# Performance work log

Hardware: AMD Instinct MI355X
Metric: run time of the kernel (lower is better)

## Reference

```python
import jax, jax.numpy as jnp
import numpy as np

V, E, H1, H2, B, T = 50000, 256, 512, 512, 512, 80

def setup_inputs() -> dict:
    key = jax.random.key(0)
    ks = jax.random.split(key, 10)
    s = lambda fan: 1.0 / np.sqrt(fan)
    return {
        "tokens": jax.random.randint(ks[0], (B, T), 0, V),
        "emb": jax.random.normal(ks[1], (V, E), jnp.float32) * 0.05,
        "W1": jax.random.normal(ks[2], (E, 4 * H1), jnp.float32) * s(E),
        "U1": jax.random.normal(ks[3], (H1, 4 * H1), jnp.float32) * s(H1),
        "b1": jnp.zeros((4 * H1,), jnp.float32),
        "W2": jax.random.normal(ks[4], (H1, 4 * H2), jnp.float32) * s(H1),
        "U2": jax.random.normal(ks[5], (H2, 4 * H2), jnp.float32) * s(H2),
        "b2": jnp.zeros((4 * H2,), jnp.float32),
        "Wfc": jax.random.normal(ks[6], (H2, 1), jnp.float32) * s(H2),
        "bfc": jnp.zeros((1,), jnp.float32),
    }

def _lstm_step(x, h, c, W, U, b):
    # z: [B, 4H] in Keras gate order i, f, g(cell), o
    z = x @ W + h @ U + b
    i, f, g, o = jnp.split(z, 4, axis=-1)
    c_new = jax.nn.sigmoid(f) * c + jax.nn.sigmoid(i) * jnp.tanh(g)
    h_new = jax.nn.sigmoid(o) * jnp.tanh(c_new)
    return h_new, c_new

def reference(tokens, emb, W1, U1, b1, W2, U2, b2, Wfc, bfc):
    X = emb[tokens]                    # [B, T, E]
    Xt = jnp.swapaxes(X, 0, 1)         # [T, B, E] for scan over time
    Bsz = tokens.shape[0]
    init = (jnp.zeros((Bsz, H1), X.dtype), jnp.zeros((Bsz, H1), X.dtype),
            jnp.zeros((Bsz, H2), X.dtype), jnp.zeros((Bsz, H2), X.dtype))

    def step(carry, x):
        h1, c1, h2, c2 = carry
        h1, c1 = _lstm_step(x, h1, c1, W1, U1, b1)
        h2, c2 = _lstm_step(h1, h2, c2, W2, U2, b2)
        return (h1, c1, h2, c2), None

    (h1, c1, h2, c2), _ = jax.lax.scan(step, init, Xt)
    # Dense(1) on last-step layer-2 output, then sigmoid (dropout inactive at inference)
    return jax.nn.sigmoid(h2 @ Wfc + bfc)   # [B, 1]
```

## Files before the change

### kernel.cpp

```cpp
#include <hip/hip_runtime.h>
#include <hip/hip_bf16.h>

typedef __bf16  bf16x8 __attribute__((ext_vector_type(8)));
typedef float   f32x4  __attribute__((ext_vector_type(4)));

#define GLOAD16_C(gptr, lptr) \
  __builtin_amdgcn_global_load_lds((const __attribute__((address_space(1))) void*)(gptr), \
                                   (__attribute__((address_space(3))) void*)(lptr), 16, 0, 0)
#define GLOAD16_H(gptr, lptr) \
  __builtin_amdgcn_global_load_lds((const __attribute__((address_space(1))) void*)(gptr), \
                                   (__attribute__((address_space(3))) void*)(lptr), 16, 0, 0x1)

#define WAIT_VM10  asm volatile("s_waitcnt vmcnt(10)" ::: "memory")
#define WAIT_VM8   asm volatile("s_waitcnt vmcnt(8)"  ::: "memory")
#define WAIT_VM6   asm volatile("s_waitcnt vmcnt(6)"  ::: "memory")
#define WAIT_VM4   asm volatile("s_waitcnt vmcnt(4)"  ::: "memory")
#define WAIT_VM2   asm volatile("s_waitcnt vmcnt(2)"  ::: "memory")
#define WAIT_VM0   asm volatile("s_waitcnt vmcnt(0)"  ::: "memory")

__device__ __forceinline__ void wait_vm_chunks(int n) {
  if      (n <= 0) WAIT_VM0;
  else if (n == 1) WAIT_VM2;
  else if (n == 2) WAIT_VM4;
  else if (n == 3) WAIT_VM6;
  else if (n == 4) WAIT_VM8;
  else             WAIT_VM10;
}
__device__ __forceinline__ void wait_lgkm_n(int n) {
  if      (n <= 0) asm volatile("s_waitcnt lgkmcnt(0)" ::: "memory");
  else if (n <= 2) asm volatile("s_waitcnt lgkmcnt(2)" ::: "memory");
  else             asm volatile("s_waitcnt lgkmcnt(6)" ::: "memory");
}

__device__ __forceinline__ float sigm(float x)  { return 1.0f / (1.0f + __expf(-x)); }
__device__ __forceinline__ float tanhp(float x) { return 2.0f / (1.0f + __expf(-2.0f * x)) - 1.0f; }

__device__ __forceinline__ unsigned int coh_load(const unsigned int* p) {
  unsigned int v;
  asm volatile("global_load_dword %0, %1, off sc0 sc1\n\ts_waitcnt vmcnt(0)"
               : "=v"(v) : "v"(p) : "memory");
  return v;
}
__device__ __forceinline__ int coh_load_i(const int* p) {
  int v;
  asm volatile("global_load_dword %0, %1, off sc0 sc1\n\ts_waitcnt vmcnt(0)"
               : "=v"(v) : "v"(p) : "memory");
  return v;
}
__device__ __forceinline__ void coh_store16(void* p, bf16x8 v) {
  f32x4 f = *(f32x4*)&v;
  asm volatile("global_store_dwordx4 %0, %1, off sc0 sc1" :: "v"(p), "v"(f) : "memory");
}
__device__ __forceinline__ void flag_store(int* fp, int v) {
  asm volatile("global_store_dword %0, %1, off sc0 sc1" :: "v"(fp), "v"(v) : "memory");
}

#define TSTEPS 80
#define BATCH  512
#define EDIM   256
#define HDIM   512
#define K2     1024
#define K1     768
#define NCH    16
#define D_SLOTS 12
#define SLOT_BYTES 524544
#define RING_OFF 65536
#define EPI_OFF  131072
#define EPI_STR  24
#define LDS_BYTES 137216

struct Params {
  const __hip_bfloat16* Wz1t;
  const __hip_bfloat16* Wz2t;
  const float* bz1;
  const float* bz2;
  const __hip_bfloat16* Xall;
  char* h1base;
  char* h2base;
  int* flags;
  const float* Wfc; const float* bfc;
  float* out;
};


__global__ __launch_bounds__(256) void prep_weights(
    const float* __restrict__ W1, const float* __restrict__ U1, const float* __restrict__ b1,
    const float* __restrict__ W2, const float* __restrict__ U2, const float* __restrict__ b2,
    __hip_bfloat16* __restrict__ Wz1t, __hip_bfloat16* __restrict__ Wz2t,
    float* __restrict__ bz1, float* __restrict__ bz2) {
  long idx = (long)blockIdx.x * 256 + threadIdx.x;
  const long n1 = 2048L * K1, n2 = 2048L * K2;
  if (idx < n1) {
    int n = (int)(idx / K1), k = (int)(idx % K1);
    int col = ((n >> 4) & 3) * 512 + (n >> 6) * 16 + (n & 15);
    float v = (k < 256) ? W1[(size_t)k * 2048 + col] : U1[(size_t)(k - 256) * 2048 + col];
    Wz1t[idx] = __float2bfloat16(v);
  } else if (idx < n1 + n2) {
    long r = idx - n1;
    int n = (int)(r / K2), k = (int)(r % K2);
    int col = ((n >> 4) & 3) * 512 + (n >> 6) * 16 + (n & 15);
    float v = (k < 512) ? W2[(size_t)k * 2048 + col] : U2[(size_t)(k - 512) * 2048 + col];
    Wz2t[r] = __float2bfloat16(v);
  } else if (idx < n1 + n2 + 2048) {
    int n = (int)(idx - (n1 + n2));
    bz1[n] = b1[((n >> 4) & 3) * 512 + (n >> 6) * 16 + (n & 15)];
  } else if (idx < n1 + n2 + 4096) {
    int n = (int)(idx - (n1 + n2 + 2048));
    bz2[n] = b2[((n >> 4) & 3) * 512 + (n >> 6) * 16 + (n & 15)];
  }
}

__global__ __launch_bounds__(256) void prep_gather(
    const int* __restrict__ tokens, const float* __restrict__ emb,
    __hip_bfloat16* __restrict__ Xall, float4* __restrict__ zp, int zn) {
  int idx = blockIdx.x * 256 + threadIdx.x;
  if (idx < zn) zp[idx] = make_float4(0.f, 0.f, 0.f, 0.f);
  int e  = (idx & 63) * 4;
  int rb = idx >> 6;
  int t  = rb >> 9;
  int b  = rb & 511;
  int tok = tokens[b * TSTEPS + t];
  const float4 v = *(const float4*)&emb[(size_t)tok * EDIM + e];
  __hip_bfloat16* o = Xall + (size_t)rb * EDIM + e;
  o[0] = __float2bfloat16(v.x); o[1] = __float2bfloat16(v.y);
  o[2] = __float2bfloat16(v.z); o[3] = __float2bfloat16(v.w);
}


__device__ __forceinline__ void gate_wave(const int* flags, int base1, int t1,
                                          int base2, int t2, int lane) {
  const int idx = lane & 31;
  const int* fp = flags + (((lane < 32) ? base1 : base2) + idx) * 4;
  const int tgt = (lane < 32) ? t1 : t2;
  for (;;) {
    int v = coh_load_i(fp);
    if (__ballot(v >= tgt) == ~0ull) break;
    __builtin_amdgcn_s_sleep(2);
  }
}

template<int K0, int LEN, int STRIDE, bool COH>
__device__ __forceinline__ void run_part(
    const __hip_bfloat16* __restrict__ Asrc, int m0, int w, int lane,
    __hip_bfloat16* __restrict__ ring, const __hip_bfloat16* __restrict__ BsL,
    const bf16x8 (&breg)[NCH][4], const int (&aoff)[2], const int (&boff)[4],
    f32x4 (&acc)[2][4]) {
  auto stage = [&](int kc) {
#pragma unroll
    for (int it = 0; it < 2; ++it) {
      const int gbase = w * 128 + it * 64;
      const int g   = gbase + lane;
      const int row = g >> 2;
      const int gc  = (g & 3) ^ ((row >> 1) & 3);
      __hip_bfloat16* lp = ring + (kc & 7) * 4096 + gbase * 8;
      const __hip_bfloat16* gp = Asrc + (size_t)(m0 + row) * STRIDE + (kc - K0) * 32 + gc * 8;
      if (COH) GLOAD16_H(gp, lp); else GLOAD16_C(gp, lp);
    }
  };
#pragma unroll
  for (int f = 0; f < 6; ++f) stage(K0 + f);

  bf16x8 af[2][2], bf[2][4];
  wait_vm_chunks(5);
#pragma unroll
  for (int mi = 0; mi < 2; ++mi)
    af[0][mi] = *(const bf16x8*)(ring + (K0 & 7) * 4096 + aoff[mi]);
  if (K0 >= NCH)
#pragma unroll
    for (int g = 0; g < 4; ++g)
      bf[0][g] = *(const bf16x8*)(BsL + (K0 - NCH) * 2048 + boff[g]);

#pragma unroll
  for (int i = 0; i < LEN; ++i) {
    const int kc  = K0 + i;
    const int cur = i & 1, nxt = cur ^ 1;
    if (i + 1 < LEN) {
      wait_vm_chunks(LEN - 2 - i < 4 ? LEN - 2 - i : 4);
      const int kn = kc + 1;
#pragma unroll
      for (int mi = 0; mi < 2; ++mi)
        af[nxt][mi] = *(const bf16x8*)(ring + (kn & 7) * 4096 + aoff[mi]);
      if (kn >= NCH) {
#pragma unroll
        for (int g = 0; g < 4; ++g)
          bf[nxt][g] = *(const bf16x8*)(BsL + (kn - NCH) * 2048 + boff[g]);
        wait_lgkm_n(6);
      } else {
        wait_lgkm_n(2);
      }
      if (i + 6 < LEN) stage(kc + 6);
    } else {
      wait_lgkm_n(0);
    }
#pragma unroll
    for (int mi = 0; mi < 2; ++mi)
#pragma unroll
      for (int g = 0; g < 4; ++g)
        acc[mi][g] = __builtin_amdgcn_mfma_f32_16x16x32_bf16(
            af[cur][mi], (kc < NCH ? breg[kc][g] : bf[cur][g]), acc[mi][g], 0, 0, 0);
  }
}

template<bool Z2>
__device__ __forceinline__ void role_loop(const Params& p, char* smem, int tid,
                                          int grp, int ntile) {
  constexpr int K   = Z2 ? K2 : K1;
  constexpr int NC  = K / 32;
  constexpr int NCA = Z2 ? 16 : 8;
  const int lane = tid & 63;
  const int w    = tid >> 6;
  const int q    = lane >> 4;
  const int m16  = lane & 15;
  const int m0   = grp * 128;
  const int n0   = ntile * 64;

  __hip_bfloat16* BsL  = (__hip_bfloat16*)smem;
  __hip_bfloat16* ring = (__hip_bfloat16*)(smem + RING_OFF);
  __hip_bfloat16* epi  = (__hip_bfloat16*)(smem + EPI_OFF);

  const __hip_bfloat16* Bg = (Z2 ? p.Wz2t : p.Wz1t) + (size_t)n0 * K;

  bf16x8 breg[NCH][4];
#pragma unroll
  for (int kc = 0; kc < NCH; ++kc)
#pragma unroll
    for (int g = 0; g < 4; ++g)
      breg[kc][g] = *(const bf16x8*)(Bg + (size_t)(g * 16 + m16) * K + kc * 32 + q * 8);

  for (int it0 = tid; it0 < (NC - NCH) * 256; it0 += 256) {
    int cid = it0 >> 8, gg = it0 & 255;
    int r = gg >> 2, c8 = gg & 3;
    int sw = c8 ^ ((r >> 1) & 3);
    *(bf16x8*)(BsL + cid * 2048 + r * 32 + sw * 8) =
        *(const bf16x8*)(Bg + (size_t)r * K + (NCH + cid) * 32 + c8 * 8);
  }
  const float* bias = Z2 ? p.bz2 : p.bz1;
  float bz[4];
#pragma unroll
  for (int g = 0; g < 4; ++g) bz[g] = bias[n0 + g * 16 + m16];

  const int swz = (q ^ ((m16 >> 1) & 3)) * 8;
  int aoff[2], boff[4];
#pragma unroll
  for (int mi = 0; mi < 2; ++mi) aoff[mi] = (w * 32 + mi * 16 + m16) * 32 + swz;
#pragma unroll
  for (int g = 0; g < 4; ++g)    boff[g]  = (g * 16 + m16) * 32 + swz;

  float cst[2][4] = {{0.f,0.f,0.f,0.f},{0.f,0.f,0.f,0.f}};
  const int fself = (Z2 ? 128 : 0) + grp * 32 + ntile;
  const int jbase = ntile * 16;
  __syncthreads();

  for (int s = 0; s < TSTEPS; ++s) {
    const int sl = s % D_SLOTS, slp = (s + D_SLOTS - 1) % D_SLOTS;
    const __hip_bfloat16* Aa = Z2
        ? (const __hip_bfloat16*)(p.h1base + (size_t)sl * SLOT_BYTES)
        : p.Xall + (size_t)s * BATCH * EDIM;
    const __hip_bfloat16* Ab = Z2
        ? (const __hip_bfloat16*)(p.h2base + (size_t)slp * SLOT_BYTES)
        : (const __hip_bfloat16*)(p.h1base + (size_t)slp * SLOT_BYTES);
    __hip_bfloat16* hout = (__hip_bfloat16*)
        ((Z2 ? p.h2base : p.h1base) + (size_t)sl * SLOT_BYTES);

    f32x4 acc[2][4];
#pragma unroll
    for (int mi = 0; mi < 2; ++mi)
#pragma unroll
      for (int g = 0; g < 4; ++g)
        acc[mi][g] = (f32x4){bz[g], bz[g], bz[g], bz[g]};

    if (Z2) {
      if (w == 0) gate_wave(p.flags, grp * 32, s + 1, grp * 32, s + 1, lane);
      __syncthreads();
    }
    if (Z2) run_part<0, 16, 512, true >(Aa, m0, w, lane, ring, BsL, breg, aoff, boff, acc);
    else    run_part<0,  8, 256, false>(Aa, m0, w, lane, ring, BsL, breg, aoff, boff, acc);

    if (w == 0) {
      if (Z2) gate_wave(p.flags, 128 + grp * 32, s, 128 + grp * 32, s, lane);
      else    gate_wave(p.flags, grp * 32, s, 128 + grp * 32, s - (D_SLOTS - 1), lane);
      if ((s & 7) == 0) __builtin_amdgcn_fence(__ATOMIC_ACQUIRE, "agent");
    }
    __syncthreads();
    if (Z2) run_part<16, 16, 512, true>(Ab, m0, w, lane, ring, BsL, breg, aoff, boff, acc);
    else    run_part< 8, 16, 512, true>(Ab, m0, w, lane, ring, BsL, breg, aoff, boff, acc);

#pragma unroll
    for (int mi = 0; mi < 2; ++mi)
#pragma unroll
      for (int rr = 0; rr < 4; ++rr) {
        const float zi = acc[mi][0][rr], zf = acc[mi][1][rr];
        const float zg = acc[mi][2][rr], zo = acc[mi][3][rr];
        const float cn = sigm(zf) * cst[mi][rr] + sigm(zi) * tanhp(zg);
        cst[mi][rr] = cn;
        epi[(w * 32 + mi * 16 + q * 4 + rr) * EPI_STR + m16] = __float2bfloat16(sigm(zo) * tanhp(cn));
      }
    __syncthreads();
    {
      const int r = tid >> 1, hf = tid & 1;
      bf16x8 hv = *(const bf16x8*)(epi + r * EPI_STR + hf * 8);
      coh_store16(hout + (size_t)(m0 + r) * HDIM + jbase + hf * 8, hv);
    }
    WAIT_VM0;
    __syncthreads();
    if (tid == 0) flag_store(p.flags + fself * 4, s + 1);
  }
}

__global__ __launch_bounds__(256, 1) void lstm_seq(Params p) {
  extern __shared__ char smem[];
  const int tid = threadIdx.x;
  const bool z2  = ((blockIdx.x & 1) == 0);
  const int grp  = (blockIdx.x >> 1) & 3;
  const int ntile = blockIdx.x >> 3;

  if (z2) role_loop<true>(p, smem, tid, grp, ntile);
  else    role_loop<false>(p, smem, tid, grp, ntile);

  const int lane = tid & 63, w = tid >> 6;
  if (w == 0) {
    const int g2 = blockIdx.x >> 6;
    gate_wave(p.flags, 128 + g2 * 32, TSTEPS, 128 + g2 * 32, TSTEPS, lane);
  }
  __syncthreads();
  if (w < 2) {
    const int row = blockIdx.x * 2 + w;
    const unsigned int* hp = (const unsigned int*)
        (p.h2base + (size_t)((TSTEPS - 1) % D_SLOTS) * SLOT_BYTES) + (size_t)row * (HDIM / 2);
    float sum = 0.f;
#pragma unroll
    for (int cc = 0; cc < 4; ++cc) {
      unsigned int d = coh_load(hp + lane * 4 + cc);
      union { unsigned int ui; float f; } lo, hi;
      lo.ui = d << 16; hi.ui = d & 0xffff0000u;
      sum += lo.f * p.Wfc[(lane * 4 + cc) * 2] + hi.f * p.Wfc[(lane * 4 + cc) * 2 + 1];
    }
#pragma unroll
    for (int o = 32; o > 0; o >>= 1) sum += __shfl_down(sum, o, 64);
    if (lane == 0) p.out[row] = sigm(sum + p.bfc[0]);
  }
}


extern "C" void kernel_launch(void* const* d_in, const int* in_sizes, int n_in,
                              void* d_out, int out_size, void* d_ws, size_t ws_size,
                              hipStream_t stream) {
  const int*   tokens = (const int*)d_in[0];
  const float* emb = (const float*)d_in[1];
  const float* W1  = (const float*)d_in[2];
  const float* U1  = (const float*)d_in[3];
  const float* b1  = (const float*)d_in[4];
  const float* W2  = (const float*)d_in[5];
  const float* U2  = (const float*)d_in[6];
  const float* b2  = (const float*)d_in[7];
  const float* Wfc = (const float*)d_in[8];
  const float* bfc = (const float*)d_in[9];

  char* ws = (char*)d_ws;
  size_t off = 0;
  auto alloc = [&](size_t bytes) {
    char* r = ws + off;
    off += (bytes + 255) & ~(size_t)255;
    return r;
  };
  __hip_bfloat16* Wz1t = (__hip_bfloat16*)alloc(2048UL * K1 * 2);
  __hip_bfloat16* Wz2t = (__hip_bfloat16*)alloc(2048UL * K2 * 2);
  float* bz1 = (float*)alloc(2048 * 4);
  float* bz2 = (float*)alloc(2048 * 4);
  __hip_bfloat16* Xall = (__hip_bfloat16*)alloc((size_t)TSTEPS * BATCH * EDIM * 2);
  const size_t state_bytes = 24UL * SLOT_BYTES + 4096;
  char* state = alloc(state_bytes);

  Params prm;
  prm.h1base = state;
  prm.h2base = state + 12UL * SLOT_BYTES;
  prm.flags  = (int*)(state + 24UL * SLOT_BYTES);

  prep_weights<<<dim3(14352), dim3(256), 0, stream>>>(W1, U1, b1, W2, U2, b2, Wz1t, Wz2t, bz1, bz2);
  prep_gather<<<dim3(10240), dim3(256), 0, stream>>>(tokens, emb, Xall,
                                                     (float4*)state, (int)(state_bytes / 16));

  hipFuncSetAttribute((const void*)lstm_seq,
                      hipFuncAttributeMaxDynamicSharedMemorySize, LDS_BYTES);

  prm.Wz1t = Wz1t; prm.Wz2t = Wz2t; prm.bz1 = bz1; prm.bz2 = bz2;
  prm.Xall = Xall;
  prm.Wfc = Wfc; prm.bfc = bfc;
  prm.out = (float*)d_out;

  lstm_seq<<<dim3(256), dim3(256), LDS_BYTES, stream>>>(prm);
}
```

Baseline: 715.3 us.

## Merge the two K-phase loops into one deeper prefetch pipeline per step

Replaces the two separate run_part calls (input part and recurrent part), each with its own pipeline fill and drain, with a single run_loop over all K chunks. Loads for the recurrent operand are staged right after the input operand's, and the prefetch distance grows from 6 to 7 chunks in the 8-slot ring. The layer-2 role now waits once on both the h1 and h2 flags before starting, where it used to wait twice with a barrier in between. The barrier between the epilogue's LDS writes and the cross-wave LDS reads is replaced by a local lgkm wait, which removes a block-wide sync but may introduce a race, since threads read epi rows written by other waves.

```diff
diff --git a/kernel.cpp b/kernel.cpp
--- a/kernel.cpp
+++ b/kernel.cpp
@@ -11,6 +11,7 @@
   __builtin_amdgcn_global_load_lds((const __attribute__((address_space(1))) void*)(gptr), \
                                    (__attribute__((address_space(3))) void*)(lptr), 16, 0, 0x1)
 
+#define WAIT_VM12  asm volatile("s_waitcnt vmcnt(12)" ::: "memory")
 #define WAIT_VM10  asm volatile("s_waitcnt vmcnt(10)" ::: "memory")
 #define WAIT_VM8   asm volatile("s_waitcnt vmcnt(8)"  ::: "memory")
 #define WAIT_VM6   asm volatile("s_waitcnt vmcnt(6)"  ::: "memory")
@@ -24,7 +25,8 @@
   else if (n == 2) WAIT_VM4;
   else if (n == 3) WAIT_VM6;
   else if (n == 4) WAIT_VM8;
-  else             WAIT_VM10;
+  else if (n == 5) WAIT_VM10;
+  else             WAIT_VM12;
 }
 __device__ __forceinline__ void wait_lgkm_n(int n) {
   if      (n <= 0) asm volatile("s_waitcnt lgkmcnt(0)" ::: "memory");
@@ -139,43 +141,46 @@
   }
 }
 
-template<int K0, int LEN, int STRIDE, bool COH>
-__device__ __forceinline__ void run_part(
-    const __hip_bfloat16* __restrict__ Asrc, int m0, int w, int lane,
+template<int SPLIT, int SA, int SB, bool COHA>
+__device__ __forceinline__ void stage_chunk(int kc,
+    const __hip_bfloat16* __restrict__ Aa, const __hip_bfloat16* __restrict__ Ab,
+    int m0, int w, int lane, __hip_bfloat16* __restrict__ ring) {
+#pragma unroll
+  for (int it = 0; it < 2; ++it) {
+    const int gbase = w * 128 + it * 64;
+    const int g   = gbase + lane;
+    const int row = g >> 2;
+    const int gc  = (g & 3) ^ ((row >> 1) & 3);
+    __hip_bfloat16* lp = ring + (kc & 7) * 4096 + gbase * 8;
+    if (kc < SPLIT) {
+      const __hip_bfloat16* gp = Aa + (size_t)(m0 + row) * SA + kc * 32 + gc * 8;
+      if (COHA) { GLOAD16_H(gp, lp); } else { GLOAD16_C(gp, lp); }
+    } else {
+      const __hip_bfloat16* gp = Ab + (size_t)(m0 + row) * SB + (kc - SPLIT) * 32 + gc * 8;
+      GLOAD16_H(gp, lp);
+    }
+  }
+}
+
+template<int LEN, int SPLIT, int SA, int SB, bool COHA>
+__device__ __forceinline__ void run_loop(
+    const __hip_bfloat16* __restrict__ Aa, const __hip_bfloat16* __restrict__ Ab,
+    int m0, int w, int lane,
     __hip_bfloat16* __restrict__ ring, const __hip_bfloat16* __restrict__ BsL,
     const bf16x8 (&breg)[NCH][4], const int (&aoff)[2], const int (&boff)[4],
     f32x4 (&acc)[2][4]) {
-  auto stage = [&](int kc) {
-#pragma unroll
-    for (int it = 0; it < 2; ++it) {
-      const int gbase = w * 128 + it * 64;
-      const int g   = gbase + lane;
-      const int row = g >> 2;
-      const int gc  = (g & 3) ^ ((row >> 1) & 3);
-      __hip_bfloat16* lp = ring + (kc & 7) * 4096 + gbase * 8;
-      const __hip_bfloat16* gp = Asrc + (size_t)(m0 + row) * STRIDE + (kc - K0) * 32 + gc * 8;
-      if (COH) GLOAD16_H(gp, lp); else GLOAD16_C(gp, lp);
-    }
-  };
-#pragma unroll
-  for (int f = 0; f < 6; ++f) stage(K0 + f);
-
   bf16x8 af[2][2], bf[2][4];
-  wait_vm_chunks(5);
+  wait_vm_chunks(6);
 #pragma unroll
   for (int mi = 0; mi < 2; ++mi)
-    af[0][mi] = *(const bf16x8*)(ring + (K0 & 7) * 4096 + aoff[mi]);
-  if (K0 >= NCH)
-#pragma unroll
-    for (int g = 0; g < 4; ++g)
-      bf[0][g] = *(const bf16x8*)(BsL + (K0 - NCH) * 2048 + boff[g]);
+    af[0][mi] = *(const bf16x8*)(ring + aoff[mi]);
 
 #pragma unroll
   for (int i = 0; i < LEN; ++i) {
-    const int kc  = K0 + i;
+    const int kc  = i;
     const int cur = i & 1, nxt = cur ^ 1;
     if (i + 1 < LEN) {
-      wait_vm_chunks(LEN - 2 - i < 4 ? LEN - 2 - i : 4);
+      wait_vm_chunks(LEN - 2 - i < 5 ? LEN - 2 - i : 5);
       const int kn = kc + 1;
 #pragma unroll
       for (int mi = 0; mi < 2; ++mi)
@@ -188,7 +193,7 @@
       } else {
         wait_lgkm_n(2);
       }
-      if (i + 6 < LEN) stage(kc + 6);
+      if (i + 7 < LEN) stage_chunk<SPLIT, SA, SB, COHA>(kc + 7, Aa, Ab, m0, w, lane, ring);
     } else {
       wait_lgkm_n(0);
     }
@@ -206,7 +211,6 @@
                                           int grp, int ntile) {
   constexpr int K   = Z2 ? K2 : K1;
   constexpr int NC  = K / 32;
-  constexpr int NCA = Z2 ? 16 : 8;
   const int lane = tid & 63;
   const int w    = tid >> 6;
   const int q    = lane >> 4;
@@ -269,21 +273,27 @@
       for (int g = 0; g < 4; ++g)
         acc[mi][g] = (f32x4){bz[g], bz[g], bz[g], bz[g]};
 
-    if (Z2) {
-      if (w == 0) gate_wave(p.flags, grp * 32, s + 1, grp * 32, s + 1, lane);
-      __syncthreads();
-    }
-    if (Z2) run_part<0, 16, 512, true >(Aa, m0, w, lane, ring, BsL, breg, aoff, boff, acc);
-    else    run_part<0,  8, 256, false>(Aa, m0, w, lane, ring, BsL, breg, aoff, boff, acc);
+    if (!Z2) {
+#pragma unroll
+      for (int f = 0; f < 7; ++f)
+        stage_chunk<8, EDIM, HDIM, false>(f, Aa, Ab, m0, w, lane, ring);
+    }
 
     if (w == 0) {
-      if (Z2) gate_wave(p.flags, 128 + grp * 32, s, 128 + grp * 32, s, lane);
+      if (Z2) gate_wave(p.flags, grp * 32, s + 1, 128 + grp * 32, s, lane);
       else    gate_wave(p.flags, grp * 32, s, 128 + grp * 32, s - (D_SLOTS - 1), lane);
       if ((s & 7) == 0) __builtin_amdgcn_fence(__ATOMIC_ACQUIRE, "agent");
     }
     __syncthreads();
-    if (Z2) run_part<16, 16, 512, true>(Ab, m0, w, lane, ring, BsL, breg, aoff, boff, acc);
-    else    run_part< 8, 16, 512, true>(Ab, m0, w, lane, ring, BsL, breg, aoff, boff, acc);
+
+    if (Z2) {
+#pragma unroll
+      for (int f = 0; f < 7; ++f)
+        stage_chunk<16, HDIM, HDIM, true>(f, Aa, Ab, m0, w, lane, ring);
+      run_loop<32, 16, HDIM, HDIM, true >(Aa, Ab, m0, w, lane, ring, BsL, breg, aoff, boff, acc);
+    } else {
+      run_loop<24,  8, EDIM, HDIM, false>(Aa, Ab, m0, w, lane, ring, BsL, breg, aoff, boff, acc);
+    }
 
 #pragma unroll
     for (int mi = 0; mi < 2; ++mi)
@@ -295,7 +305,7 @@
         cst[mi][rr] = cn;
         epi[(w * 32 + mi * 16 + q * 4 + rr) * EPI_STR + m16] = __float2bfloat16(sigm(zo) * tanhp(cn));
       }
-    __syncthreads();
+    wait_lgkm_n(0);
     {
       const int r = tid >> 1, hf = tid & 1;
       bf16x8 hv = *(const bf16x8*)(epi + r * EPI_STR + hf * 8);
```

Result: slower. 789.9 us (+10.4%).

## Prefetch next timestep's input chunks before publishing the step flag

Applied to the files above, without the earlier changes.

Each step's first input chunks are now loaded into the LDS ring during the previous step's epilogue, right after the h store and before the completion flag is published. For layer 2 this also moves the wait on layer-1 flags ahead of that prefetch. The in-loop prefetch depth grows from 6 to 7 chunks, with matching vmcnt thresholds, and the barrier between the epilogue LDS write and its cross-wave read is replaced by a per-wave lgkmcnt wait. The aim is to hide global-load latency across the serial recurrence. The risks are possible cross-wave races: on the epilogue staging buffer, and on ring slots that waves may still be reading while the next step's prefetch overwrites them.

```diff
diff --git a/kernel.cpp b/kernel.cpp
--- a/kernel.cpp
+++ b/kernel.cpp
@@ -11,6 +11,8 @@
   __builtin_amdgcn_global_load_lds((const __attribute__((address_space(1))) void*)(gptr), \
                                    (__attribute__((address_space(3))) void*)(lptr), 16, 0, 0x1)
 
+#define WAIT_VM14  asm volatile("s_waitcnt vmcnt(14)" ::: "memory")
+#define WAIT_VM12  asm volatile("s_waitcnt vmcnt(12)" ::: "memory")
 #define WAIT_VM10  asm volatile("s_waitcnt vmcnt(10)" ::: "memory")
 #define WAIT_VM8   asm volatile("s_waitcnt vmcnt(8)"  ::: "memory")
 #define WAIT_VM6   asm volatile("s_waitcnt vmcnt(6)"  ::: "memory")
@@ -24,7 +26,8 @@
   else if (n == 2) WAIT_VM4;
   else if (n == 3) WAIT_VM6;
   else if (n == 4) WAIT_VM8;
-  else             WAIT_VM10;
+  else if (n == 5) WAIT_VM10;
+  else             WAIT_VM12;
 }
 __device__ __forceinline__ void wait_lgkm_n(int n) {
   if      (n <= 0) asm volatile("s_waitcnt lgkmcnt(0)" ::: "memory");
@@ -139,29 +142,34 @@
   }
 }
 
-template<int K0, int LEN, int STRIDE, bool COH>
+template<int STRIDE, bool COH>
+__device__ __forceinline__ void stage_one(const __hip_bfloat16* __restrict__ A,
+    int kc, int kcol, int m0, int w, int lane, __hip_bfloat16* __restrict__ ring) {
+#pragma unroll
+  for (int it = 0; it < 2; ++it) {
+    const int gbase = w * 128 + it * 64;
+    const int g   = gbase + lane;
+    const int row = g >> 2;
+    const int gc  = (g & 3) ^ ((row >> 1) & 3);
+    __hip_bfloat16* lp = ring + (kc & 7) * 4096 + gbase * 8;
+    const __hip_bfloat16* gp = A + (size_t)(m0 + row) * STRIDE + kcol * 32 + gc * 8;
+    if (COH) { GLOAD16_H(gp, lp); } else { GLOAD16_C(gp, lp); }
+  }
+}
+
+template<int K0, int LEN, int STRIDE, bool COH, bool PREFILLED>
 __device__ __forceinline__ void run_part(
-    const __hip_bfloat16* __restrict__ Asrc, int m0, int w, int lane,
+    const __hip_bfloat16* __restrict__ A, int m0, int w, int lane,
     __hip_bfloat16* __restrict__ ring, const __hip_bfloat16* __restrict__ BsL,
     const bf16x8 (&breg)[NCH][4], const int (&aoff)[2], const int (&boff)[4],
     f32x4 (&acc)[2][4]) {
-  auto stage = [&](int kc) {
-#pragma unroll
-    for (int it = 0; it < 2; ++it) {
-      const int gbase = w * 128 + it * 64;
-      const int g   = gbase + lane;
-      const int row = g >> 2;
-      const int gc  = (g & 3) ^ ((row >> 1) & 3);
-      __hip_bfloat16* lp = ring + (kc & 7) * 4096 + gbase * 8;
-      const __hip_bfloat16* gp = Asrc + (size_t)(m0 + row) * STRIDE + (kc - K0) * 32 + gc * 8;
-      if (COH) GLOAD16_H(gp, lp); else GLOAD16_C(gp, lp);
-    }
-  };
-#pragma unroll
-  for (int f = 0; f < 6; ++f) stage(K0 + f);
-
+  if (!PREFILLED) {
+#pragma unroll
+    for (int f = 0; f < 7; ++f)
+      stage_one<STRIDE, COH>(A, K0 + f, f, m0, w, lane, ring);
+  }
   bf16x8 af[2][2], bf[2][4];
-  wait_vm_chunks(5);
+  wait_vm_chunks(6);
 #pragma unroll
   for (int mi = 0; mi < 2; ++mi)
     af[0][mi] = *(const bf16x8*)(ring + (K0 & 7) * 4096 + aoff[mi]);
@@ -175,7 +183,7 @@
     const int kc  = K0 + i;
     const int cur = i & 1, nxt = cur ^ 1;
     if (i + 1 < LEN) {
-      wait_vm_chunks(LEN - 2 - i < 4 ? LEN - 2 - i : 4);
+      wait_vm_chunks(LEN - 2 - i < 5 ? LEN - 2 - i : 5);
       const int kn = kc + 1;
 #pragma unroll
       for (int mi = 0; mi < 2; ++mi)
@@ -188,7 +196,7 @@
       } else {
         wait_lgkm_n(2);
       }
-      if (i + 6 < LEN) stage(kc + 6);
+      if (i + 7 < LEN) stage_one<STRIDE, COH>(A, kc + 7, i + 7, m0, w, lane, ring);
     } else {
       wait_lgkm_n(0);
     }
@@ -206,7 +214,7 @@
                                           int grp, int ntile) {
   constexpr int K   = Z2 ? K2 : K1;
   constexpr int NC  = K / 32;
-  constexpr int NCA = Z2 ? 16 : 8;
+  constexpr int LENA = Z2 ? 16 : 8;
   const int lane = tid & 63;
   const int w    = tid >> 6;
   const int q    = lane >> 4;
@@ -250,6 +258,19 @@
   const int fself = (Z2 ? 128 : 0) + grp * 32 + ntile;
   const int jbase = ntile * 16;
   __syncthreads();
+
+  if (Z2) {
+    if (w == 0) gate_wave(p.flags, grp * 32, 1, grp * 32, 1, lane);
+    __syncthreads();
+  }
+  {
+    const __hip_bfloat16* A0 = Z2
+        ? (const __hip_bfloat16*)p.h1base
+        : p.Xall;
+#pragma unroll
+    for (int f = 0; f < 7; ++f)
+      stage_one<(Z2 ? HDIM : EDIM), Z2>(A0, f, f, m0, w, lane, ring);
+  }
 
   for (int s = 0; s < TSTEPS; ++s) {
     const int sl = s % D_SLOTS, slp = (s + D_SLOTS - 1) % D_SLOTS;
@@ -269,12 +290,8 @@
       for (int g = 0; g < 4; ++g)
         acc[mi][g] = (f32x4){bz[g], bz[g], bz[g], bz[g]};
 
-    if (Z2) {
-      if (w == 0) gate_wave(p.flags, grp * 32, s + 1, grp * 32, s + 1, lane);
-      __syncthreads();
-    }
-    if (Z2) run_part<0, 16, 512, true >(Aa, m0, w, lane, ring, BsL, breg, aoff, boff, acc);
-    else    run_part<0,  8, 256, false>(Aa, m0, w, lane, ring, BsL, breg, aoff, boff, acc);
+    if (Z2) run_part<0, 16, HDIM, true,  true>(Aa, m0, w, lane, ring, BsL, breg, aoff, boff, acc);
+    else    run_part<0,  8, EDIM, false, true>(Aa, m0, w, lane, ring, BsL, breg, aoff, boff, acc);
 
     if (w == 0) {
       if (Z2) gate_wave(p.flags, 128 + grp * 32, s, 128 + grp * 32, s, lane);
@@ -282,8 +299,9 @@
       if ((s & 7) == 0) __builtin_amdgcn_fence(__ATOMIC_ACQUIRE, "agent");
     }
     __syncthreads();
-    if (Z2) run_part<16, 16, 512, true>(Ab, m0, w, lane, ring, BsL, breg, aoff, boff, acc);
-    else    run_part< 8, 16, 512, true>(Ab, m0, w, lane, ring, BsL, breg, aoff, boff, acc);
+
+    if (Z2) run_part<16, 16, HDIM, true, false>(Ab, m0, w, lane, ring, BsL, breg, aoff, boff, acc);
+    else    run_part< 8, 16, HDIM, true, false>(Ab, m0, w, lane, ring, BsL, breg, aoff, boff, acc);
 
 #pragma unroll
     for (int mi = 0; mi < 2; ++mi)
@@ -295,15 +313,36 @@
         cst[mi][rr] = cn;
         epi[(w * 32 + mi * 16 + q * 4 + rr) * EPI_STR + m16] = __float2bfloat16(sigm(zo) * tanhp(cn));
       }
-    __syncthreads();
+    wait_lgkm_n(0);
     {
       const int r = tid >> 1, hf = tid & 1;
       bf16x8 hv = *(const bf16x8*)(epi + r * EPI_STR + hf * 8);
       coh_store16(hout + (size_t)(m0 + r) * HDIM + jbase + hf * 8, hv);
     }
-    WAIT_VM0;
-    __syncthreads();
-    if (tid == 0) flag_store(p.flags + fself * 4, s + 1);
+
+    if (s + 1 < TSTEPS) {
+      if (Z2) {
+        if (w == 0) gate_wave(p.flags, grp * 32, s + 2, grp * 32, s + 2, lane);
+        __syncthreads();
+        const __hip_bfloat16* An =
+            (const __hip_bfloat16*)(p.h1base + (size_t)((s + 1) % D_SLOTS) * SLOT_BYTES);
+#pragma unroll
+        for (int f = 0; f < 7; ++f)
+          stage_one<HDIM, true>(An, f, f, m0, w, lane, ring);
+      } else {
+        const __hip_bfloat16* An = p.Xall + (size_t)(s + 1) * BATCH * EDIM;
+#pragma unroll
+        for (int f = 0; f < 7; ++f)
+          stage_one<EDIM, false>(An, f, f, m0, w, lane, ring);
+      }
+      WAIT_VM14;
+      __syncthreads();
+      if (tid == 0) flag_store(p.flags + fself * 4, s + 1);
+    } else {
+      WAIT_VM0;
+      __syncthreads();
+      if (tid == 0) flag_store(p.flags + fself * 4, s + 1);
+    }
   }
 }
 
```

Result: slower. 730.6 us (+2.1%).
